# Performance work log

Hardware: AMD Instinct MI355X
Metric: run time of the kernel (lower is better)

The kernel has to match this reference:

```python
import jax, jax.numpy as jnp
import numpy as np

WS = 7          # window_size (square)
HEADS = 12


def _relative_position_index(ws=WS):
    # Faithful port of WindowAttentionBase._get_relative_position_index
    coords = np.stack(np.meshgrid(np.arange(ws), np.arange(ws), indexing='ij'))  # [2, ws, ws]
    flat = coords.reshape(2, -1)                       # [2, n]
    rel = flat[:, :, None] - flat[:, None, :]          # [2, n, n]
    rel = rel.transpose(1, 2, 0)                       # [n, n, 2]
    rel[:, :, 0] += ws - 1
    rel[:, :, 1] += ws - 1
    rel[:, :, 0] *= 2 * ws - 1
    return jnp.asarray(rel.sum(-1).reshape(-1), dtype=jnp.int32)  # [n*n]


def setup_inputs() -> dict:
    key = jax.random.key(0)
    ks = jax.random.split(key, 6)
    b, H, W, c = 32, 56, 56, 384
    return {
        "x": jax.random.normal(ks[0], (b, H, W, c), jnp.float32),
        "w_qkv": jax.random.normal(ks[1], (3 * c, c), jnp.float32) * (c ** -0.5),
        "b_qkv": jax.random.normal(ks[2], (3 * c,), jnp.float32) * 0.02,
        "rel_pos": jax.random.normal(ks[3], (HEADS, (2 * WS - 1) ** 2), jnp.float32),
        "w_out": jax.random.normal(ks[4], (c, c), jnp.float32) * (c ** -0.5),
        "b_out": jax.random.normal(ks[5], (c,), jnp.float32) * 0.02,
    }


def reference(x, w_qkv, b_qkv, rel_pos, w_out, b_out):
    b, H, W, c = x.shape
    g = HEADS
    d = c // g
    hn, wn = H // WS, W // WS
    n = WS * WS
    scale = d ** -0.5

    # split_into_windows: 'b (p h) (q w) c -> b h w (p q) c'  (p,q = window dims, OUTER factors)
    xw = x.reshape(b, WS, hn, WS, wn, c).transpose(0, 2, 4, 1, 3, 5).reshape(b, hn, wn, n, c)

    qkv = xw @ w_qkv.T + b_qkv                          # [b, hn, wn, n, 3c]
    q, k, v = jnp.split(qkv, 3, axis=-1)
    # 'b h w n (g d) -> b g h w n d'
    to_heads = lambda t: t.reshape(b, hn, wn, n, g, d).transpose(0, 4, 1, 2, 3, 5)
    q, k, v = to_heads(q) * scale, to_heads(k), to_heads(v)

    sim = jnp.einsum('bghwnd,bghwmd->bghwnm', q, k)     # [b, g, hn, wn, n, n]
    idx = _relative_position_index()
    bias = rel_pos[:, idx].reshape(g, n, n)             # gather relative position bias
    sim = sim + bias[None, :, None, None, :, :]

    attn = jax.nn.softmax(sim, axis=-1)
    out = jnp.einsum('bghwnm,bghwmd->bghwnd', attn, v)  # [b, g, hn, wn, n, d]

    # 'b g h w n d -> b h w n (g d)' then merge_windows 'b h w (p q) c -> b (p h) (q w) c'
    out = out.transpose(0, 2, 3, 4, 1, 5).reshape(b, hn, wn, n, c)
    out = out.reshape(b, hn, wn, WS, WS, c).transpose(0, 3, 1, 4, 2, 5).reshape(b, H, W, c)
    return out @ w_out.T + b_out
```

## Files before the change

kernel.cpp:

```cpp
#include <hip/hip_runtime.h>

typedef __attribute__((ext_vector_type(8))) short bf16x8;
typedef __attribute__((ext_vector_type(4))) float f32x4;

__device__ __forceinline__ unsigned short f2bf(float f){
  unsigned u = __builtin_bit_cast(unsigned, f);
  u += 0x7fffu + ((u >> 16) & 1u);
  return (unsigned short)(u >> 16);
}

__device__ __forceinline__ unsigned cvt_pk_bf16(float lo, float hi){
  unsigned r;
  asm("v_cvt_pk_bf16_f32 %0, %1, %2" : "=v"(r) : "v"(lo), "v"(hi));
  return r;
}

#define ASYNC16(ldsp, gp) __builtin_amdgcn_global_load_lds( \
    (const __attribute__((address_space(1))) unsigned int*)(gp), \
    (__attribute__((address_space(3))) unsigned int*)(ldsp), 16, 0, 0)

__global__ __launch_bounds__(256) void prep_kernel(const float* __restrict__ x,
                                                   const float* __restrict__ wq,
                                                   const float* __restrict__ wo,
                                                   const float* __restrict__ rel_pos,
                                                   unsigned short* __restrict__ xb,
                                                   unsigned short* __restrict__ wqb,
                                                   unsigned short* __restrict__ wob,
                                                   float* __restrict__ btab){
  const int bid = blockIdx.x;
  if (bid < 37632){
    int idx = bid*256 + threadIdx.x;
    int token = idx / 96, j = idx - token*96;
    int b = token / 3136, rem = token - b*3136;
    int rr = rem / 56, cp = rem - rr*56;
    int p = rr >> 3, h = rr & 7, q = cp >> 3, w = cp & 7;
    int orow = ((b*8 + h)*8 + w)*49 + p*7 + q;
    float4 v = *(const float4*)(x + (size_t)idx*4);
    ushort4 o;
    o.x = f2bf(v.x); o.y = f2bf(v.y); o.z = f2bf(v.z); o.w = f2bf(v.w);
    *(ushort4*)(xb + (size_t)orow*384 + j*4) = o;
  } else if (bid < 37992){
    int idx = (bid - 37632)*256 + threadIdx.x;
    if (idx < 55296){
      int lane = idx & 63;
      int r = idx >> 6;
      int wt = r & 7; int r2 = r >> 3;
      int t = r2 % 12, gi = r2 / 12;
      int hgp = gi / 3, m = gi - hgp*3;
      int row = m*384 + hgp*128 + (wt>>1)*32 + (wt&1)*16 + (lane & 15);
      int col = t*32 + (lane >> 4)*8;
      const float* s = wq + (size_t)row*384 + col;
      float4 v1 = *(const float4*)(s);
      float4 v2 = *(const float4*)(s + 4);
      ushort4 o1, o2;
      o1.x=f2bf(v1.x); o1.y=f2bf(v1.y); o1.z=f2bf(v1.z); o1.w=f2bf(v1.w);
      o2.x=f2bf(v2.x); o2.y=f2bf(v2.y); o2.z=f2bf(v2.z); o2.w=f2bf(v2.w);
      unsigned short* dst = wqb + (size_t)idx*8;
      *(ushort4*)(dst)     = o1;
      *(ushort4*)(dst + 4) = o2;
    } else {
      int k = idx - 55296;
      float4 v = *(const float4*)(wo + (size_t)k*4);
      ushort4 o; o.x=f2bf(v.x); o.y=f2bf(v.y); o.z=f2bf(v.z); o.w=f2bf(v.w);
      *(ushort4*)(wob + (size_t)k*4) = o;
    }
  } else {
    int idx = (bid - 37992)*256 + threadIdx.x;
    int head = idx >> 10, rem = idx & 1023;
    int fi = rem >> 6, lane = rem & 63;
    int ti = fi >> 2, tj = fi & 3;
    int qq = tj*16 + (lane & 15);
    int kb = ti*16 + (lane >> 4)*4;
    float4 v; float* vp = (float*)&v;
#pragma unroll
    for (int r=0; r<4; ++r){
      int kk = kb + r;
      float val;
      if (kk >= 49) val = -__builtin_inff();
      else if (qq >= 49) val = 0.f;
      else {
        int ip = qq/7, iq = qq - ip*7, jp = kk/7, jq = kk - jp*7;
        val = rel_pos[head*169 + (ip-jp+6)*13 + (iq-jq+6)] * 1.4426950408889634f;
      }
      vp[r] = val;
    }
    *(float4*)(btab + (size_t)idx*4) = v;
  }
}

__global__ __launch_bounds__(256, 2) void fqa_kernel(const unsigned short* __restrict__ xb,
                                                     const unsigned short* __restrict__ Wf,
                                                     const float* __restrict__ bqkv,
                                                     const float* __restrict__ btab,
                                                     unsigned short* __restrict__ ao)
{
  __shared__ unsigned short QK[4][4096];
  __shared__ unsigned short VT[4][2048];
  __shared__ unsigned short P [4][4096];
  const int tid = threadIdx.x, lane = tid & 63, wid = tid >> 6;
  const int l15 = lane & 15, kg = lane >> 4;
  const int win = blockIdx.x & 2047;
  const int hg  = blockIdx.x >> 11;
  const int head = hg*4 + wid;

  const unsigned short* ap[4];
#pragma unroll
  for (int ti=0; ti<4; ++ti){
    int rowg = win*49 + ti*16 + l15;
    if (rowg > 100351) rowg = 100351;
    ap[ti] = xb + (size_t)rowg*384 + kg*8;
  }
  const unsigned short* bp[3][2];
#pragma unroll
  for (int m=0; m<3; ++m)
#pragma unroll
    for (int tjj=0; tjj<2; ++tjj)
      bp[m][tjj] = Wf + ((size_t)((hg*3 + m)*12)*8 + wid*2 + tjj)*512 + lane*8;

  f32x4 aq[4][2] = {}, ak[4][2] = {}, av[4][2] = {};
  bf16x8 afr[2][4], bq[2][2], bk[2][2], bv[2][2];

#define LOADA(d, t) do { \
    afr[d][0] = *(const bf16x8*)(ap[0] + (t)*32); \
    afr[d][1] = *(const bf16x8*)(ap[1] + (t)*32); \
    afr[d][2] = *(const bf16x8*)(ap[2] + (t)*32); \
    afr[d][3] = *(const bf16x8*)(ap[3] + (t)*32); \
  } while(0)
#define LOADB(d, t) do { \
    bq[d][0] = *(const bf16x8*)(bp[0][0] + (t)*4096); \
    bq[d][1] = *(const bf16x8*)(bp[0][1] + (t)*4096); \
    bk[d][0] = *(const bf16x8*)(bp[1][0] + (t)*4096); \
    bk[d][1] = *(const bf16x8*)(bp[1][1] + (t)*4096); \
    bv[d][0] = *(const bf16x8*)(bp[2][0] + (t)*4096); \
    bv[d][1] = *(const bf16x8*)(bp[2][1] + (t)*4096); \
  } while(0)

  LOADA(0, 0); LOADB(0, 0);
#pragma unroll
  for (int t=0; t<12; ++t){
    const int cur = t & 1;
    if (t < 11){ LOADA(cur^1, t+1); LOADB(cur^1, t+1); }
    __builtin_amdgcn_s_setprio(1);
#pragma unroll
    for (int ti=0; ti<4; ++ti)
#pragma unroll
      for (int tjj=0; tjj<2; ++tjj){
        aq[ti][tjj] = __builtin_amdgcn_mfma_f32_16x16x32_bf16(afr[cur][ti], bq[cur][tjj], aq[ti][tjj], 0,0,0);
        ak[ti][tjj] = __builtin_amdgcn_mfma_f32_16x16x32_bf16(afr[cur][ti], bk[cur][tjj], ak[ti][tjj], 0,0,0);
        av[ti][tjj] = __builtin_amdgcn_mfma_f32_16x16x32_bf16(afr[cur][ti], bv[cur][tjj], av[ti][tjj], 0,0,0);
      }
    __builtin_amdgcn_s_setprio(0);
  }
#undef LOADA
#undef LOADB

  const float SCL = 0.17677669529663689f * 1.4426950408889634f;
  float biasq[2], biask[2], biasv[2];
#pragma unroll
  for (int tjj=0; tjj<2; ++tjj){
    int col = hg*128 + wid*32 + tjj*16 + l15;
    biasq[tjj] = bqkv[col] * SCL;
    biask[tjj] = bqkv[384 + col];
    biasv[tjj] = bqkv[768 + col];
  }

  unsigned short* QKl = QK[wid];
  unsigned short* VTl = VT[wid];
#pragma unroll
  for (int ti=0; ti<4; ++ti){
#pragma unroll
    for (int tjj=0; tjj<2; ++tjj){
      const int cq = tjj*2 + (l15 >> 3);
      const int ck = 4 + tjj*2 + (l15 >> 3);
      const int sub = (l15 & 7)*2;
#pragma unroll
      for (int r=0; r<4; ++r){
        int tok = ti*16 + kg*4 + r;
        unsigned oq = (unsigned)(tok*128 + ((cq ^ (tok & 7)) << 4) + sub);
        unsigned ok = (unsigned)(tok*128 + ((ck ^ (tok & 7)) << 4) + sub);
        *(unsigned short*)((char*)QKl + oq) = f2bf(aq[ti][tjj][r]*SCL + biasq[tjj]);
        *(unsigned short*)((char*)QKl + ok) = f2bf(ak[ti][tjj][r] + biask[tjj]);
      }
      int dd = tjj*16 + l15;
      int cb = ti*2 + (kg >> 1);
      uint2 d;
      d.x = cvt_pk_bf16(av[ti][tjj][0] + biasv[tjj], av[ti][tjj][1] + biasv[tjj]);
      d.y = cvt_pk_bf16(av[ti][tjj][2] + biasv[tjj], av[ti][tjj][3] + biasv[tjj]);
      unsigned ov = (unsigned)(dd*128 + ((cb ^ (dd & 7)) << 4) + (kg & 1)*8);
      *(uint2*)((char*)VTl + ov) = d;
    }
  }

  const float* bt = btab + head*4096;
  f32x4 s[4][4];
#pragma unroll
  for (int ti=0; ti<4; ++ti)
#pragma unroll
    for (int tj=0; tj<4; ++tj)
      s[ti][tj] = *(const f32x4*)(bt + ((ti*4 + tj)*64 + lane)*4);

  bf16x8 kf[4], qf[4];
#pragma unroll
  for (int i=0; i<4; ++i){
    int tok = i*16 + l15;
    qf[i] = *(const bf16x8*)((char*)QKl + tok*128 + ((kg       ^ (tok & 7)) << 4));
    kf[i] = *(const bf16x8*)((char*)QKl + tok*128 + (((4 + kg) ^ (tok & 7)) << 4));
  }

  __builtin_amdgcn_s_setprio(1);
#pragma unroll
  for (int ti=0; ti<4; ++ti)
#pragma unroll
    for (int tj=0; tj<4; ++tj)
      s[ti][tj] = __builtin_amdgcn_mfma_f32_16x16x32_bf16(kf[ti], qf[tj], s[ti][tj], 0,0,0);
  __builtin_amdgcn_s_setprio(0);

  float rinv[4];
#pragma unroll
  for (int tj=0; tj<4; ++tj){
    float sum = 0.f;
#pragma unroll
    for (int ti=0; ti<4; ++ti)
#pragma unroll
      for (int r=0; r<4; ++r){
        float e = exp2f(s[ti][tj][r]);
        s[ti][tj][r] = e;
        sum += e;
      }
    sum += __shfl_xor(sum, 16);
    sum += __shfl_xor(sum, 32);
    rinv[tj] = __builtin_amdgcn_rcpf(sum);
  }

  unsigned short* Pl = P[wid];
  const unsigned swzP = (unsigned)((l15 & 7) << 4);
#pragma unroll
  for (int tj=0; tj<4; ++tj){
    const float rv = rinv[tj];
    const unsigned rowb = (unsigned)((tj*16 + l15)*128);
#pragma unroll
    for (int ti=0; ti<4; ++ti){
      uint2 d;
      d.x = cvt_pk_bf16(s[ti][tj][0]*rv, s[ti][tj][1]*rv);
      d.y = cvt_pk_bf16(s[ti][tj][2]*rv, s[ti][tj][3]*rv);
      unsigned boff = (rowb + (unsigned)(ti*32 + kg*8)) ^ swzP;
      *(uint2*)((char*)Pl + boff) = d;
    }
  }

  bf16x8 vfk[2][2];
#pragma unroll
  for (int ks=0; ks<2; ++ks)
#pragma unroll
    for (int tjv=0; tjv<2; ++tjv){
      int dd = tjv*16 + l15;
      vfk[ks][tjv] = *(const bf16x8*)((char*)VTl + dd*128 + (((ks*4 + kg) ^ (dd & 7)) << 4));
    }

  f32x4 o[4][2] = {};
#pragma unroll
  for (int oti=0; oti<4; ++oti){
    bf16x8 pa[2];
#pragma unroll
    for (int ks=0; ks<2; ++ks){
      unsigned boff = ((unsigned)((oti*16 + l15)*128 + ks*64 + kg*16)) ^ swzP;
      pa[ks] = *(const bf16x8*)((char*)Pl + boff);
    }
    __builtin_amdgcn_s_setprio(1);
#pragma unroll
    for (int tjv=0; tjv<2; ++tjv){
      o[oti][tjv] = __builtin_amdgcn_mfma_f32_16x16x32_bf16(pa[0], vfk[0][tjv], o[oti][tjv], 0,0,0);
      o[oti][tjv] = __builtin_amdgcn_mfma_f32_16x16x32_bf16(pa[1], vfk[1][tjv], o[oti][tjv], 0,0,0);
    }
    __builtin_amdgcn_s_setprio(0);
  }

#pragma unroll
  for (int oti=0; oti<4; ++oti)
#pragma unroll
    for (int r=0; r<4; ++r){
      int row = oti*16 + kg*4 + r;
      if (row < 49){
        unsigned short* op = ao + ((size_t)win*49 + row)*384 + head*32 + l15;
        op[0]  = (unsigned short)cvt_pk_bf16(o[oti][0][r], o[oti][0][r]);
        op[16] = (unsigned short)cvt_pk_bf16(o[oti][1][r], o[oti][1][r]);
      }
    }
}

template<int NBY>
__global__ __launch_bounds__(256) void gemm256(const unsigned short* __restrict__ A,
                                               const unsigned short* __restrict__ B,
                                               const float* __restrict__ bias,
                                               float* __restrict__ out)
{
  constexpr int K = 384;
  constexpr int NT = 12;
  __shared__ unsigned short Al[3][256*32];
  __shared__ unsigned short Bl[3][128*32];
  const int tid = threadIdx.x;
  const int lane = tid & 63, wid = tid >> 6;
  const int wr = wid >> 1, wc = wid & 1;
  const int l15 = lane & 15, kg = lane >> 4;
  const int swz = (l15 >> 1) & 3;
  const int cswz = (tid & 3) ^ ((tid >> 3) & 3);

  const int n = blockIdx.x;
  const int xcd = n & 7, s = n >> 3;
  const int panel = s / NBY, nb = s - panel*NBY;
  const int bx = panel*8 + xcd, by = nb;

  const unsigned short* Ag = A + ((size_t)bx*256 + (tid>>2))*K + cswz*8;
  const unsigned short* Bg = B + ((size_t)(by*128 + (tid>>2)))*K + cswz*8;

  f32x4 acc[8][4] = {};

#define STAGE(buf, kt) do { \
    ASYNC16(&Al[buf][wid*512],        Ag + (kt)*32); \
    ASYNC16(&Al[buf][wid*512 + 2048], Ag + (size_t)64*K  + (kt)*32); \
    ASYNC16(&Al[buf][wid*512 + 4096], Ag + (size_t)128*K + (kt)*32); \
    ASYNC16(&Al[buf][wid*512 + 6144], Ag + (size_t)192*K + (kt)*32); \
    ASYNC16(&Bl[buf][wid*512],        Bg + (kt)*32); \
    ASYNC16(&Bl[buf][wid*512 + 2048], Bg + (size_t)64*K  + (kt)*32); \
  } while(0)

  STAGE(0,0); STAGE(1,1);

#pragma unroll
  for (int t = 0; t < NT; ++t){
    if (t < NT-1) asm volatile("s_waitcnt vmcnt(6)\n\ts_barrier" ::: "memory");
    else          asm volatile("s_waitcnt vmcnt(0)\n\ts_barrier" ::: "memory");

    if (t + 2 < NT) STAGE((t+2)%3, t+2);

    const unsigned short* Ab = Al[t % 3];
    const unsigned short* Bb = Bl[t % 3];
    bf16x8 af[8], bfv[4];
#pragma unroll
    for (int ti=0; ti<8; ++ti)
      af[ti] = *(const bf16x8*)(Ab + (wr*128 + ti*16 + l15)*32 + (kg ^ swz)*8);
#pragma unroll
    for (int tj=0; tj<4; ++tj)
      bfv[tj] = *(const bf16x8*)(Bb + (wc*64 + tj*16 + l15)*32 + (kg ^ swz)*8);

    __builtin_amdgcn_s_setprio(1);
#pragma unroll
    for (int ti=0; ti<8; ++ti)
#pragma unroll
      for (int tj=0; tj<4; ++tj)
        acc[ti][tj] = __builtin_amdgcn_mfma_f32_16x16x32_bf16(af[ti], bfv[tj], acc[ti][tj], 0,0,0);
    __builtin_amdgcn_s_setprio(0);
  }
#undef STAGE

  const int rbase = bx*256 + wr*128 + kg*4;
  const int cbs = by*128 + wc*64;
  float bv[4];
#pragma unroll
  for (int tj=0; tj<4; ++tj) bv[tj] = bias[cbs + tj*16 + l15];
#pragma unroll
  for (int ti=0; ti<8; ++ti){
#pragma unroll
    for (int r=0; r<4; ++r){
      int R = rbase + ti*16 + r;
      int win = R / 49, nn = R - win*49;
      int p = nn / 7, q = nn - p*7;
      int h = (win >> 3) & 7, w = win & 7;
      size_t tok = (size_t)(win >> 6)*3136 + (size_t)((p*8 + h)*56 + q*8 + w);
      float* __restrict__ orow = out + tok*384 + cbs + l15;
#pragma unroll
      for (int tj=0; tj<4; ++tj)
        orow[tj*16] = acc[ti][tj][r] + bv[tj];
    }
  }
}

extern "C" void kernel_launch(void* const* d_in, const int* in_sizes, int n_in,
                              void* d_out, int out_size, void* d_ws, size_t ws_size,
                              hipStream_t stream)
{
  const float* x       = (const float*)d_in[0];
  const float* w_qkv   = (const float*)d_in[1];
  const float* b_qkv   = (const float*)d_in[2];
  const float* rel_pos = (const float*)d_in[3];
  const float* w_out   = (const float*)d_in[4];
  const float* b_out   = (const float*)d_in[5];
  float* out = (float*)d_out;

  char* ws = (char*)d_ws;
  unsigned short* wqb = (unsigned short*)ws;
  unsigned short* wob = (unsigned short*)(ws + 884736);
  float* btab         = (float*)(ws + 884736 + 294912);
  unsigned short* xb  = (unsigned short*)(ws + 1376256);
  unsigned short* ao  = xb + 38535168;

  prep_kernel<<<dim3(38040), dim3(256), 0, stream>>>(x, w_qkv, w_out, rel_pos,
                                                     xb, wqb, wob, btab);
  fqa_kernel<<<dim3(6144), dim3(256), 0, stream>>>(xb, wqb, b_qkv, btab, ao);
  gemm256<3><<<dim3(1176), dim3(256), 0, stream>>>(ao, wob, b_out, out);
}
```

Baseline: 306.6 us.

## Stage shared QKV input tiles in LDS via async loads and alias P onto QK

Previously each of the four waves loaded the same 64x32 slice of the window's input rows from global memory on every k-step. Now each thread issues one async global-to-LDS load, so the block fetches the slice once into a triple-buffered LDS tile, and the waves read their MFMA A fragments from swizzled LDS. A wait plus a block barrier per k-step orders the staged data. Separately, the softmax P buffer now reuses the per-wave QK region, which cuts LDS per block and helps fit two blocks per CU. The cost is a barrier in every k-step and reliance on the QK data being dead before P is written.

```diff
diff --git a/kernel.cpp b/kernel.cpp
--- a/kernel.cpp
+++ b/kernel.cpp
@@ -94,22 +94,23 @@
                                                      const float* __restrict__ btab,
                                                      unsigned short* __restrict__ ao)
 {
+  __shared__ unsigned short Al[3][2048];
   __shared__ unsigned short QK[4][4096];
   __shared__ unsigned short VT[4][2048];
-  __shared__ unsigned short P [4][4096];
   const int tid = threadIdx.x, lane = tid & 63, wid = tid >> 6;
   const int l15 = lane & 15, kg = lane >> 4;
   const int win = blockIdx.x & 2047;
   const int hg  = blockIdx.x >> 11;
   const int head = hg*4 + wid;
 
-  const unsigned short* ap[4];
-#pragma unroll
-  for (int ti=0; ti<4; ++ti){
-    int rowg = win*49 + ti*16 + l15;
-    if (rowg > 100351) rowg = 100351;
-    ap[ti] = xb + (size_t)rowg*384 + kg*8;
-  }
+  {
+  }
+  int srowg = win*49 + (tid >> 2);
+  if (srowg > 100351) srowg = 100351;
+  const int cswz = (tid & 3) ^ ((tid >> 3) & 3);
+  const unsigned short* AgS = xb + (size_t)srowg*384 + cswz*8;
+  const int rswz = (l15 >> 1) & 3;
+
   const unsigned short* bp[3][2];
 #pragma unroll
   for (int m=0; m<3; ++m)
@@ -118,14 +119,9 @@
       bp[m][tjj] = Wf + ((size_t)((hg*3 + m)*12)*8 + wid*2 + tjj)*512 + lane*8;
 
   f32x4 aq[4][2] = {}, ak[4][2] = {}, av[4][2] = {};
-  bf16x8 afr[2][4], bq[2][2], bk[2][2], bv[2][2];
-
-#define LOADA(d, t) do { \
-    afr[d][0] = *(const bf16x8*)(ap[0] + (t)*32); \
-    afr[d][1] = *(const bf16x8*)(ap[1] + (t)*32); \
-    afr[d][2] = *(const bf16x8*)(ap[2] + (t)*32); \
-    afr[d][3] = *(const bf16x8*)(ap[3] + (t)*32); \
-  } while(0)
+  bf16x8 bq[2][2], bk[2][2], bv[2][2];
+
+#define STAGE_A(buf, t) ASYNC16(&Al[buf][wid*512], AgS + (t)*32)
 #define LOADB(d, t) do { \
     bq[d][0] = *(const bf16x8*)(bp[0][0] + (t)*4096); \
     bq[d][1] = *(const bf16x8*)(bp[0][1] + (t)*4096); \
@@ -135,23 +131,37 @@
     bv[d][1] = *(const bf16x8*)(bp[2][1] + (t)*4096); \
   } while(0)
 
-  LOADA(0, 0); LOADB(0, 0);
-#pragma unroll
-  for (int t=0; t<12; ++t){
+  STAGE_A(0, 0);
+  LOADB(0, 0);
+  STAGE_A(1, 1);
+
+#pragma unroll
+  for (int t = 0; t < 12; ++t){
+    if (t < 11) asm volatile("s_waitcnt vmcnt(1)\n\ts_barrier" ::: "memory");
+    else        asm volatile("s_waitcnt vmcnt(0)\n\ts_barrier" ::: "memory");
+
+    if (t < 11)  LOADB((t+1)&1, t+1);
+    if (t < 10)  STAGE_A((t+2)%3, t+2);
+
+    const unsigned short* Ab = Al[t % 3];
+    bf16x8 afr[4];
+#pragma unroll
+    for (int ti=0; ti<4; ++ti)
+      afr[ti] = *(const bf16x8*)(Ab + (ti*16 + l15)*32 + ((kg ^ rswz)*8));
+
     const int cur = t & 1;
-    if (t < 11){ LOADA(cur^1, t+1); LOADB(cur^1, t+1); }
     __builtin_amdgcn_s_setprio(1);
 #pragma unroll
     for (int ti=0; ti<4; ++ti)
 #pragma unroll
       for (int tjj=0; tjj<2; ++tjj){
-        aq[ti][tjj] = __builtin_amdgcn_mfma_f32_16x16x32_bf16(afr[cur][ti], bq[cur][tjj], aq[ti][tjj], 0,0,0);
-        ak[ti][tjj] = __builtin_amdgcn_mfma_f32_16x16x32_bf16(afr[cur][ti], bk[cur][tjj], ak[ti][tjj], 0,0,0);
-        av[ti][tjj] = __builtin_amdgcn_mfma_f32_16x16x32_bf16(afr[cur][ti], bv[cur][tjj], av[ti][tjj], 0,0,0);
+        aq[ti][tjj] = __builtin_amdgcn_mfma_f32_16x16x32_bf16(afr[ti], bq[cur][tjj], aq[ti][tjj], 0,0,0);
+        ak[ti][tjj] = __builtin_amdgcn_mfma_f32_16x16x32_bf16(afr[ti], bk[cur][tjj], ak[ti][tjj], 0,0,0);
+        av[ti][tjj] = __builtin_amdgcn_mfma_f32_16x16x32_bf16(afr[ti], bv[cur][tjj], av[ti][tjj], 0,0,0);
       }
     __builtin_amdgcn_s_setprio(0);
   }
-#undef LOADA
+#undef STAGE_A
 #undef LOADB
 
   const float SCL = 0.17677669529663689f * 1.4426950408889634f;
@@ -232,7 +242,7 @@
     rinv[tj] = __builtin_amdgcn_rcpf(sum);
   }
 
-  unsigned short* Pl = P[wid];
+  unsigned short* Pl = QKl;
   const unsigned swzP = (unsigned)((l15 & 7) << 4);
 #pragma unroll
   for (int tj=0; tj<4; ++tj){
```

Result: faster. 278.1 us (-9.3%).
